# Kernel tuning notes

Hardware: AMD Instinct MI355X
Metric: run time of the kernel (lower is better)

The kernel has to match this reference:

```python
import jax, jax.numpy as jnp
import numpy as np

N_ACTIVE = 100000
C = 64
N_BLOCKS = 2
K = 27  # 3x3x3 submanifold rulebook offsets
BN_EPS = 1e-4  # scn BatchNorm default eps


def setup_inputs() -> dict:
    key = jax.random.key(0)
    k1, k2, k3 = jax.random.split(key, 3)
    feats = jax.random.normal(k1, (N_ACTIVE, C), dtype=jnp.float32)
    # rulebook: index N_ACTIVE == missing neighbor (points at padded zero row)
    nbrs = jax.random.randint(k2, (N_ACTIVE, K), 0, N_ACTIVE + 1, dtype=jnp.int32)
    # make the center offset (k=13) point at self, as in a real submanifold rulebook
    nbrs = nbrs.at[:, K // 2].set(jnp.arange(N_ACTIVE, dtype=jnp.int32))
    fan_in = K * C
    W = jax.random.normal(k3, (N_BLOCKS, 2, K, C, C), dtype=jnp.float32) / np.sqrt(fan_in)
    gamma = jnp.ones((N_BLOCKS, 2, C), dtype=jnp.float32)
    beta = jnp.zeros((N_BLOCKS, 2, C), dtype=jnp.float32)
    return {"feats": feats, "nbrs": nbrs, "W": W, "gamma": gamma, "beta": beta}


def _subm_conv(x, nbrs, Wk):
    # x: [N, C]; nbrs: [N, K] with value N meaning 'missing'; Wk: [K, C, C]
    x_pad = jnp.concatenate([x, jnp.zeros((1, x.shape[1]), x.dtype)], axis=0)
    g = x_pad[nbrs]  # [N, K, C] rulebook gather
    return jnp.einsum('nkc,kcd->nd', g, Wk)  # gather-GEMM-scatter fused by contraction


def _bn(x, g, b):
    mu = jnp.mean(x, axis=0)
    var = jnp.var(x, axis=0)
    return (x - mu) * jax.lax.rsqrt(var + BN_EPS) * g + b


def reference(feats, nbrs, W, gamma, beta):
    x = feats
    for i in range(N_BLOCKS):  # SparseResidualBlock chain
        residual = x
        out = _subm_conv(x, nbrs, W[i, 0])
        out = jax.nn.relu(_bn(out, gamma[i, 0], beta[i, 0]))  # BatchNormReLU
        out = _subm_conv(out, nbrs, W[i, 1])
        out = _bn(out, gamma[i, 1], beta[i, 1])  # BatchNormalization
        x = jax.nn.relu(out + residual)  # AddTable + ReLU
    return x
```

## Files before the change

### kernel.cpp

```cpp
#include <hip/hip_runtime.h>

#define N_PTS 100000
#define NT_STRIDE 100096
#define NK 27
#define TOTAL (N_PTS * 64)
#define NB_CONV 782

typedef short bf16x8 __attribute__((ext_vector_type(8)));
typedef float f32x4 __attribute__((ext_vector_type(4)));
typedef unsigned short u16x8 __attribute__((ext_vector_type(8)));

__device__ __forceinline__ unsigned short f2bf(float f) {
    unsigned u = __builtin_bit_cast(unsigned, f);
    u += 0x7fffu + ((u >> 16) & 1u);
    return (unsigned short)(u >> 16);
}
__device__ __forceinline__ float bf2f(unsigned short u) {
    return __builtin_bit_cast(float, ((unsigned)u) << 16);
}

__global__ void cast_in_k(const float* __restrict__ feats, unsigned short* __restrict__ xb) {
    int t = blockIdx.x * 256 + threadIdx.x;
    if (t >= (N_PTS + 1) * 8) return;
    int i = t * 8;
    u16x8 o;
    if (i < TOTAL) {
        f32x4 v0 = ((const f32x4*)(feats + i))[0];
        f32x4 v1 = ((const f32x4*)(feats + i))[1];
#pragma unroll
        for (int j = 0; j < 4; ++j) { o[j] = f2bf(v0[j]); o[4 + j] = f2bf(v1[j]); }
    } else {
#pragma unroll
        for (int j = 0; j < 8; ++j) o[j] = 0;
    }
    *(u16x8*)(xb + i) = o;
}

__global__ void tr_nbrs_k(const int* __restrict__ nbrs, int* __restrict__ nbrsT) {
    __shared__ int tile[64 * 28];
    const int n0 = blockIdx.x * 64;
    const int t = threadIdx.x;
    const int base = n0 * 27;
    for (int i = t; i < 1728; i += 256) {
        int v = (base + i < N_PTS * 27) ? nbrs[base + i] : N_PTS;
        int r = i / 27, c = i - r * 27;
        tile[r * 28 + c] = v;
    }
    __syncthreads();
    for (int i = t; i < 1728; i += 256) {
        int k = i >> 6, j = i & 63;
        nbrsT[(size_t)k * NT_STRIDE + n0 + j] = tile[j * 28 + k];
    }
}

__global__ void pack_w_k(const float* __restrict__ W, unsigned short* __restrict__ Wp) {
    int o = blockIdx.x * 256 + threadIdx.x;
    if (o >= 4 * NK * 4096) return;
    int conv = o / (NK * 4096);
    int r = o - conv * (NK * 4096);
    int k = r >> 12;
    int r2 = r & 4095;
    int frag = r2 >> 9;
    int kk = frag >> 2, cb = frag & 3;
    int lane = (r2 >> 3) & 63;
    int j = r2 & 7;
    int c = kk * 32 + (lane >> 4) * 8 + j;
    int d = cb * 16 + (lane & 15);
    Wp[o] = f2bf(W[(size_t)(conv * NK + k) * 4096 + c * 64 + d]);
}

__global__ __launch_bounds__(256, 3) void conv_k(
    const unsigned short* __restrict__ xb,
    const int* __restrict__ nbrsT,
    const unsigned short* __restrict__ Wp,
    unsigned short* __restrict__ ybf,
    float* __restrict__ partials)
{
    const int tid = threadIdx.x;
    const int lane = tid & 63;
    const int wave = tid >> 6;
    const int l15 = lane & 15;
    const int lgrp = lane >> 4;
    const int wave_row = blockIdx.x * 128 + wave * 32;
    const int r0 = wave_row + l15;
    const int r1 = r0 + 16;

    f32x4 acc[2][4];
#pragma unroll
    for (int m = 0; m < 2; ++m)
#pragma unroll
        for (int cb = 0; cb < 4; ++cb) acc[m][cb] = (f32x4)0.f;

    const bf16x8* wp = (const bf16x8*)Wp;

    int id0[4], id1[4];
#pragma unroll
    for (int s = 0; s < 4; ++s) {
        id0[s] = nbrsT[(size_t)s * NT_STRIDE + r0];
        id1[s] = nbrsT[(size_t)s * NT_STRIDE + r1];
    }
    bf16x8 apf[3][4];
#pragma unroll
    for (int s = 0; s < 2; ++s) {
        const bf16x8* p0 = (const bf16x8*)(xb + (size_t)id0[s] * 64);
        const bf16x8* p1 = (const bf16x8*)(xb + (size_t)id1[s] * 64);
        apf[s][0] = p0[lgrp]; apf[s][1] = p0[4 + lgrp];
        apf[s][2] = p1[lgrp]; apf[s][3] = p1[4 + lgrp];
    }

#pragma unroll
    for (int k = 0; k < NK; ++k) {
        if (k + 4 < NK) {
            id0[k & 3] = nbrsT[(size_t)(k + 4) * NT_STRIDE + r0];
            id1[k & 3] = nbrsT[(size_t)(k + 4) * NT_STRIDE + r1];
        }
        if (k + 2 < NK) {
            const int j = (k + 2) & 3;
            const int s2 = (k + 2) % 3;
            const bf16x8* p0 = (const bf16x8*)(xb + (size_t)id0[j] * 64);
            const bf16x8* p1 = (const bf16x8*)(xb + (size_t)id1[j] * 64);
            apf[s2][0] = p0[lgrp]; apf[s2][1] = p0[4 + lgrp];
            apf[s2][2] = p1[lgrp]; apf[s2][3] = p1[4 + lgrp];
        }
        const int s = k % 3;
        const bf16x8* wk = wp + (size_t)k * 512 + lane;
        {
            bf16x8 b0 = wk[0], b1 = wk[64], b2 = wk[128], b3 = wk[192];
            acc[0][0] = __builtin_amdgcn_mfma_f32_16x16x32_bf16(apf[s][0], b0, acc[0][0], 0, 0, 0);
            acc[1][0] = __builtin_amdgcn_mfma_f32_16x16x32_bf16(apf[s][2], b0, acc[1][0], 0, 0, 0);
            acc[0][1] = __builtin_amdgcn_mfma_f32_16x16x32_bf16(apf[s][0], b1, acc[0][1], 0, 0, 0);
            acc[1][1] = __builtin_amdgcn_mfma_f32_16x16x32_bf16(apf[s][2], b1, acc[1][1], 0, 0, 0);
            acc[0][2] = __builtin_amdgcn_mfma_f32_16x16x32_bf16(apf[s][0], b2, acc[0][2], 0, 0, 0);
            acc[1][2] = __builtin_amdgcn_mfma_f32_16x16x32_bf16(apf[s][2], b2, acc[1][2], 0, 0, 0);
            acc[0][3] = __builtin_amdgcn_mfma_f32_16x16x32_bf16(apf[s][0], b3, acc[0][3], 0, 0, 0);
            acc[1][3] = __builtin_amdgcn_mfma_f32_16x16x32_bf16(apf[s][2], b3, acc[1][3], 0, 0, 0);
        }
        {
            bf16x8 b0 = wk[256], b1 = wk[320], b2 = wk[384], b3 = wk[448];
            acc[0][0] = __builtin_amdgcn_mfma_f32_16x16x32_bf16(apf[s][1], b0, acc[0][0], 0, 0, 0);
            acc[1][0] = __builtin_amdgcn_mfma_f32_16x16x32_bf16(apf[s][3], b0, acc[1][0], 0, 0, 0);
            acc[0][1] = __builtin_amdgcn_mfma_f32_16x16x32_bf16(apf[s][1], b1, acc[0][1], 0, 0, 0);
            acc[1][1] = __builtin_amdgcn_mfma_f32_16x16x32_bf16(apf[s][3], b1, acc[1][1], 0, 0, 0);
            acc[0][2] = __builtin_amdgcn_mfma_f32_16x16x32_bf16(apf[s][1], b2, acc[0][2], 0, 0, 0);
            acc[1][2] = __builtin_amdgcn_mfma_f32_16x16x32_bf16(apf[s][3], b2, acc[1][2], 0, 0, 0);
            acc[0][3] = __builtin_amdgcn_mfma_f32_16x16x32_bf16(apf[s][1], b3, acc[0][3], 0, 0, 0);
            acc[1][3] = __builtin_amdgcn_mfma_f32_16x16x32_bf16(apf[s][3], b3, acc[1][3], 0, 0, 0);
        }
    }

    __shared__ __align__(16) unsigned short yt[4][32 * 72];
    unsigned short* myt = &yt[wave][0];
#pragma unroll
    for (int m = 0; m < 2; ++m)
#pragma unroll
        for (int cb = 0; cb < 4; ++cb)
#pragma unroll
            for (int r = 0; r < 4; ++r)
                myt[(m * 16 + lgrp * 4 + r) * 72 + cb * 16 + l15] = f2bf(acc[m][cb][r]);
#pragma unroll
    for (int c2 = 0; c2 < 4; ++c2) {
        int chunk = c2 * 64 + lane;
        int row = chunk >> 3;
        int col8 = chunk & 7;
        int grow = wave_row + row;
        if (grow < N_PTS) {
            u16x8 v = *(const u16x8*)(myt + row * 72 + col8 * 8);
            *(u16x8*)(ybf + (size_t)grow * 64 + col8 * 8) = v;
        }
    }

    __shared__ float sred[4][128];
#pragma unroll
    for (int cb = 0; cb < 4; ++cb) {
        float s = 0.f, s2 = 0.f;
#pragma unroll
        for (int m = 0; m < 2; ++m)
#pragma unroll
            for (int r = 0; r < 4; ++r) {
                float v = acc[m][cb][r];
                s += v; s2 += v * v;
            }
        s += __shfl_xor(s, 16); s += __shfl_xor(s, 32);
        s2 += __shfl_xor(s2, 16); s2 += __shfl_xor(s2, 32);
        if (lane < 16) {
            sred[wave][cb * 16 + l15] = s;
            sred[wave][64 + cb * 16 + l15] = s2;
        }
    }
    __syncthreads();
    if (tid < 128) {
        float p = sred[0][tid] + sred[1][tid] + sred[2][tid] + sred[3][tid];
        partials[(size_t)blockIdx.x * 128 + tid] = p;
    }
}

__global__ void bn_fin_k(const float* __restrict__ partials,
                         const float* __restrict__ gamma,
                         const float* __restrict__ beta,
                         float* __restrict__ scsh) {
    const int c = blockIdx.x;
    const int t = threadIdx.x;
    float s = 0.f, s2 = 0.f;
    for (int w = t; w < NB_CONV; w += 256) {
        s  += partials[(size_t)w * 128 + c];
        s2 += partials[(size_t)w * 128 + 64 + c];
    }
#pragma unroll
    for (int off = 1; off < 64; off <<= 1) {
        s  += __shfl_xor(s, off, 64);
        s2 += __shfl_xor(s2, off, 64);
    }
    __shared__ float sm[8];
    int wv = t >> 6, ln = t & 63;
    if (ln == 0) { sm[wv] = s; sm[4 + wv] = s2; }
    __syncthreads();
    if (t == 0) {
        float S  = sm[0] + sm[1] + sm[2] + sm[3];
        float S2 = sm[4] + sm[5] + sm[6] + sm[7];
        const float invN = 1.0f / (float)N_PTS;
        float mu = S * invN;
        float var = S2 * invN - mu * mu;
        float sc = gamma[c] * rsqrtf(var + 1e-4f);
        scsh[c] = sc;
        scsh[64 + c] = beta[c] - mu * sc;
    }
}

__global__ void bn_relu_cast_k(const unsigned short* __restrict__ ybf, const float* __restrict__ scsh,
                               unsigned short* __restrict__ xb) {
    int t = blockIdx.x * 256 + threadIdx.x;
    if (t >= TOTAL / 8) return;
    int i = t * 8;
    int c0 = i & 63;
    u16x8 v = *(const u16x8*)(ybf + i);
    f32x4 sa = *(const f32x4*)(scsh + c0);
    f32x4 sb = *(const f32x4*)(scsh + c0 + 4);
    f32x4 ba = *(const f32x4*)(scsh + 64 + c0);
    f32x4 bb = *(const f32x4*)(scsh + 64 + c0 + 4);
    u16x8 o;
#pragma unroll
    for (int j = 0; j < 4; ++j) {
        o[j]     = f2bf(fmaxf(bf2f(v[j])     * sa[j] + ba[j], 0.f));
        o[4 + j] = f2bf(fmaxf(bf2f(v[4 + j]) * sb[j] + bb[j], 0.f));
    }
    *(u16x8*)(xb + i) = o;
}

__global__ void bn_add_relu_k(const unsigned short* __restrict__ ybf, const float* __restrict__ scsh,
                              const float* __restrict__ res, float* __restrict__ xout,
                              unsigned short* __restrict__ xb, int writeBf) {
    int t = blockIdx.x * 256 + threadIdx.x;
    if (t >= TOTAL / 8) return;
    int i = t * 8;
    int c0 = i & 63;
    u16x8 v = *(const u16x8*)(ybf + i);
    f32x4 q0 = ((const f32x4*)(res + i))[0];
    f32x4 q1 = ((const f32x4*)(res + i))[1];
    f32x4 sa = *(const f32x4*)(scsh + c0);
    f32x4 sb = *(const f32x4*)(scsh + c0 + 4);
    f32x4 ba = *(const f32x4*)(scsh + 64 + c0);
    f32x4 bb = *(const f32x4*)(scsh + 64 + c0 + 4);
    f32x4 o0, o1;
#pragma unroll
    for (int j = 0; j < 4; ++j) {
        o0[j] = fmaxf(bf2f(v[j])     * sa[j] + ba[j] + q0[j], 0.f);
        o1[j] = fmaxf(bf2f(v[4 + j]) * sb[j] + bb[j] + q1[j], 0.f);
    }
    ((f32x4*)(xout + i))[0] = o0;
    ((f32x4*)(xout + i))[1] = o1;
    if (writeBf) {
        u16x8 o;
#pragma unroll
        for (int j = 0; j < 4; ++j) { o[j] = f2bf(o0[j]); o[4 + j] = f2bf(o1[j]); }
        *(u16x8*)(xb + i) = o;
    }
}

extern "C" void kernel_launch(void* const* d_in, const int* in_sizes, int n_in,
                              void* d_out, int out_size, void* d_ws, size_t ws_size,
                              hipStream_t stream) {
    const float* feats = (const float*)d_in[0];
    const int*   nbrs  = (const int*)d_in[1];
    const float* W     = (const float*)d_in[2];
    const float* gamma = (const float*)d_in[3];
    const float* beta  = (const float*)d_in[4];
    float* out = (float*)d_out;

    char* ws = (char*)d_ws;
    unsigned short* xb       = (unsigned short*)ws;
    unsigned short* ybf      = (unsigned short*)(ws + 12800512);
    unsigned short* Wp       = (unsigned short*)(ws + 25600512);
    int*            nbrsT    = (int*)(ws + 26485248);
    float*          partials = (float*)(ws + 37295616);
    float*          scsh     = (float*)(ws + 37696000);

    dim3 b256(256);
    cast_in_k<<<((N_PTS + 1) * 8 + 255) / 256, b256, 0, stream>>>(feats, xb);
    tr_nbrs_k<<<NT_STRIDE / 64, b256, 0, stream>>>(nbrs, nbrsT);
    pack_w_k<<<(4 * NK * 4096) / 256, b256, 0, stream>>>(W, Wp);

    const int appl_blocks = (TOTAL / 8) / 256;
    for (int blk = 0; blk < 2; ++blk) {
        int c0 = blk * 2, c1 = blk * 2 + 1;
        conv_k<<<NB_CONV, b256, 0, stream>>>(xb, nbrsT, Wp + (size_t)c0 * NK * 4096, ybf, partials);
        bn_fin_k<<<64, b256, 0, stream>>>(partials, gamma + c0 * 64, beta + c0 * 64, scsh);
        bn_relu_cast_k<<<appl_blocks, b256, 0, stream>>>(ybf, scsh, xb);
        conv_k<<<NB_CONV, b256, 0, stream>>>(xb, nbrsT, Wp + (size_t)c1 * NK * 4096, ybf, partials);
        bn_fin_k<<<64, b256, 0, stream>>>(partials, gamma + c1 * 64, beta + c1 * 64, scsh);
        const float* res = (blk == 0) ? feats : (const float*)out;
        bn_add_relu_k<<<appl_blocks, b256, 0, stream>>>(ybf, scsh, res, out, xb, blk == 0 ? 1 : 0);
    }
}
```

Measured before the change: 470.3 us.

## Split conv K-offsets across wave pairs with LDS reduction of partial sums

The conv kernel now gives each block 64 rows instead of 128, and splits the 27 offsets (padded to 28 with a zero weight slice and a missing-neighbor index row) between two wave pairs of 14 each. The two partial accumulators are combined through an fp32 LDS tile, after which all threads write bf16 output and compute the per-channel BN partial sums via shuffles. This doubles the grid and shortens each wave's serial gather/MFMA chain to expose more parallelism and latency hiding. In exchange it adds one padded offset of wasted work, extra LDS traffic and barriers, and twice as many partials for the BN finalize step. It also raises the launch-bounds occupancy hint and inserts a sched_barrier in the loop.

```diff
diff --git a/kernel.cpp b/kernel.cpp
--- a/kernel.cpp
+++ b/kernel.cpp
@@ -3,8 +3,9 @@
 #define N_PTS 100000
 #define NT_STRIDE 100096
 #define NK 27
+#define NKP 28
 #define TOTAL (N_PTS * 64)
-#define NB_CONV 782
+#define NB_CONV 1564
 
 typedef short bf16x8 __attribute__((ext_vector_type(8)));
 typedef float f32x4 __attribute__((ext_vector_type(4)));
@@ -51,14 +52,17 @@
         int k = i >> 6, j = i & 63;
         nbrsT[(size_t)k * NT_STRIDE + n0 + j] = tile[j * 28 + k];
     }
+    for (int i = t; i < 64; i += 256)
+        nbrsT[(size_t)27 * NT_STRIDE + n0 + i] = N_PTS;
 }
 
 __global__ void pack_w_k(const float* __restrict__ W, unsigned short* __restrict__ Wp) {
     int o = blockIdx.x * 256 + threadIdx.x;
-    if (o >= 4 * NK * 4096) return;
-    int conv = o / (NK * 4096);
-    int r = o - conv * (NK * 4096);
+    if (o >= 4 * NKP * 4096) return;
+    int conv = o / (NKP * 4096);
+    int r = o - conv * (NKP * 4096);
     int k = r >> 12;
+    if (k == 27) { Wp[o] = 0; return; }
     int r2 = r & 4095;
     int frag = r2 >> 9;
     int kk = frag >> 2, cb = frag & 3;
@@ -69,7 +73,7 @@
     Wp[o] = f2bf(W[(size_t)(conv * NK + k) * 4096 + c * 64 + d]);
 }
 
-__global__ __launch_bounds__(256, 3) void conv_k(
+__global__ __launch_bounds__(256, 4) void conv_k(
     const unsigned short* __restrict__ xb,
     const int* __restrict__ nbrsT,
     const unsigned short* __restrict__ Wp,
@@ -81,9 +85,12 @@
     const int wave = tid >> 6;
     const int l15 = lane & 15;
     const int lgrp = lane >> 4;
-    const int wave_row = blockIdx.x * 128 + wave * 32;
+    const int h = wave & 1;
+    const int kh = wave >> 1;
+    const int wave_row = blockIdx.x * 64 + h * 32;
     const int r0 = wave_row + l15;
     const int r1 = r0 + 16;
+    const int k0 = kh * 14;
 
     f32x4 acc[2][4];
 #pragma unroll
@@ -96,8 +103,8 @@
     int id0[4], id1[4];
 #pragma unroll
     for (int s = 0; s < 4; ++s) {
-        id0[s] = nbrsT[(size_t)s * NT_STRIDE + r0];
-        id1[s] = nbrsT[(size_t)s * NT_STRIDE + r1];
+        id0[s] = nbrsT[(size_t)(k0 + s) * NT_STRIDE + r0];
+        id1[s] = nbrsT[(size_t)(k0 + s) * NT_STRIDE + r1];
     }
     bf16x8 apf[3][4];
 #pragma unroll
@@ -109,82 +116,106 @@
     }
 
 #pragma unroll
-    for (int k = 0; k < NK; ++k) {
-        if (k + 4 < NK) {
-            id0[k & 3] = nbrsT[(size_t)(k + 4) * NT_STRIDE + r0];
-            id1[k & 3] = nbrsT[(size_t)(k + 4) * NT_STRIDE + r1];
-        }
-        if (k + 2 < NK) {
-            const int j = (k + 2) & 3;
-            const int s2 = (k + 2) % 3;
+    for (int s = 0; s < 14; ++s) {
+        if (s + 4 < 14) {
+            id0[s & 3] = nbrsT[(size_t)(k0 + s + 4) * NT_STRIDE + r0];
+            id1[s & 3] = nbrsT[(size_t)(k0 + s + 4) * NT_STRIDE + r1];
+        }
+        if (s + 2 < 14) {
+            const int j = (s + 2) & 3;
+            const int st = (s + 2) % 3;
             const bf16x8* p0 = (const bf16x8*)(xb + (size_t)id0[j] * 64);
             const bf16x8* p1 = (const bf16x8*)(xb + (size_t)id1[j] * 64);
-            apf[s2][0] = p0[lgrp]; apf[s2][1] = p0[4 + lgrp];
-            apf[s2][2] = p1[lgrp]; apf[s2][3] = p1[4 + lgrp];
-        }
-        const int s = k % 3;
-        const bf16x8* wk = wp + (size_t)k * 512 + lane;
+            apf[st][0] = p0[lgrp]; apf[st][1] = p0[4 + lgrp];
+            apf[st][2] = p1[lgrp]; apf[st][3] = p1[4 + lgrp];
+        }
+        __builtin_amdgcn_sched_barrier(0);
+        const int st = s % 3;
+        const bf16x8* wk = wp + (size_t)(k0 + s) * 512 + lane;
         {
             bf16x8 b0 = wk[0], b1 = wk[64], b2 = wk[128], b3 = wk[192];
-            acc[0][0] = __builtin_amdgcn_mfma_f32_16x16x32_bf16(apf[s][0], b0, acc[0][0], 0, 0, 0);
-            acc[1][0] = __builtin_amdgcn_mfma_f32_16x16x32_bf16(apf[s][2], b0, acc[1][0], 0, 0, 0);
-            acc[0][1] = __builtin_amdgcn_mfma_f32_16x16x32_bf16(apf[s][0], b1, acc[0][1], 0, 0, 0);
-            acc[1][1] = __builtin_amdgcn_mfma_f32_16x16x32_bf16(apf[s][2], b1, acc[1][1], 0, 0, 0);
-            acc[0][2] = __builtin_amdgcn_mfma_f32_16x16x32_bf16(apf[s][0], b2, acc[0][2], 0, 0, 0);
-            acc[1][2] = __builtin_amdgcn_mfma_f32_16x16x32_bf16(apf[s][2], b2, acc[1][2], 0, 0, 0);
-            acc[0][3] = __builtin_amdgcn_mfma_f32_16x16x32_bf16(apf[s][0], b3, acc[0][3], 0, 0, 0);
-            acc[1][3] = __builtin_amdgcn_mfma_f32_16x16x32_bf16(apf[s][2], b3, acc[1][3], 0, 0, 0);
+            acc[0][0] = __builtin_amdgcn_mfma_f32_16x16x32_bf16(apf[st][0], b0, acc[0][0], 0, 0, 0);
+            acc[1][0] = __builtin_amdgcn_mfma_f32_16x16x32_bf16(apf[st][2], b0, acc[1][0], 0, 0, 0);
+            acc[0][1] = __builtin_amdgcn_mfma_f32_16x16x32_bf16(apf[st][0], b1, acc[0][1], 0, 0, 0);
+            acc[1][1] = __builtin_amdgcn_mfma_f32_16x16x32_bf16(apf[st][2], b1, acc[1][1], 0, 0, 0);
+            acc[0][2] = __builtin_amdgcn_mfma_f32_16x16x32_bf16(apf[st][0], b2, acc[0][2], 0, 0, 0);
+            acc[1][2] = __builtin_amdgcn_mfma_f32_16x16x32_bf16(apf[st][2], b2, acc[1][2], 0, 0, 0);
+            acc[0][3] = __builtin_amdgcn_mfma_f32_16x16x32_bf16(apf[st][0], b3, acc[0][3], 0, 0, 0);
+            acc[1][3] = __builtin_amdgcn_mfma_f32_16x16x32_bf16(apf[st][2], b3, acc[1][3], 0, 0, 0);
         }
         {
             bf16x8 b0 = wk[256], b1 = wk[320], b2 = wk[384], b3 = wk[448];
-            acc[0][0] = __builtin_amdgcn_mfma_f32_16x16x32_bf16(apf[s][1], b0, acc[0][0], 0, 0, 0);
-            acc[1][0] = __builtin_amdgcn_mfma_f32_16x16x32_bf16(apf[s][3], b0, acc[1][0], 0, 0, 0);
-            acc[0][1] = __builtin_amdgcn_mfma_f32_16x16x32_bf16(apf[s][1], b1, acc[0][1], 0, 0, 0);
-            acc[1][1] = __builtin_amdgcn_mfma_f32_16x16x32_bf16(apf[s][3], b1, acc[1][1], 0, 0, 0);
-            acc[0][2] = __builtin_amdgcn_mfma_f32_16x16x32_bf16(apf[s][1], b2, acc[0][2], 0, 0, 0);
-            acc[1][2] = __builtin_amdgcn_mfma_f32_16x16x32_bf16(apf[s][3], b2, acc[1][2], 0, 0, 0);
-            acc[0][3] = __builtin_amdgcn_mfma_f32_16x16x32_bf16(apf[s][1], b3, acc[0][3], 0, 0, 0);
-            acc[1][3] = __builtin_amdgcn_mfma_f32_16x16x32_bf16(apf[s][3], b3, acc[1][3], 0, 0, 0);
-        }
-    }
-
-    __shared__ __align__(16) unsigned short yt[4][32 * 72];
-    unsigned short* myt = &yt[wave][0];
-#pragma unroll
-    for (int m = 0; m < 2; ++m)
-#pragma unroll
-        for (int cb = 0; cb < 4; ++cb)
-#pragma unroll
-            for (int r = 0; r < 4; ++r)
-                myt[(m * 16 + lgrp * 4 + r) * 72 + cb * 16 + l15] = f2bf(acc[m][cb][r]);
-#pragma unroll
-    for (int c2 = 0; c2 < 4; ++c2) {
-        int chunk = c2 * 64 + lane;
-        int row = chunk >> 3;
-        int col8 = chunk & 7;
-        int grow = wave_row + row;
-        if (grow < N_PTS) {
-            u16x8 v = *(const u16x8*)(myt + row * 72 + col8 * 8);
-            *(u16x8*)(ybf + (size_t)grow * 64 + col8 * 8) = v;
-        }
-    }
-
-    __shared__ float sred[4][128];
-#pragma unroll
-    for (int cb = 0; cb < 4; ++cb) {
-        float s = 0.f, s2 = 0.f;
+            acc[0][0] = __builtin_amdgcn_mfma_f32_16x16x32_bf16(apf[st][1], b0, acc[0][0], 0, 0, 0);
+            acc[1][0] = __builtin_amdgcn_mfma_f32_16x16x32_bf16(apf[st][3], b0, acc[1][0], 0, 0, 0);
+            acc[0][1] = __builtin_amdgcn_mfma_f32_16x16x32_bf16(apf[st][1], b1, acc[0][1], 0, 0, 0);
+            acc[1][1] = __builtin_amdgcn_mfma_f32_16x16x32_bf16(apf[st][3], b1, acc[1][1], 0, 0, 0);
+            acc[0][2] = __builtin_amdgcn_mfma_f32_16x16x32_bf16(apf[st][1], b2, acc[0][2], 0, 0, 0);
+            acc[1][2] = __builtin_amdgcn_mfma_f32_16x16x32_bf16(apf[st][3], b2, acc[1][2], 0, 0, 0);
+            acc[0][3] = __builtin_amdgcn_mfma_f32_16x16x32_bf16(apf[st][1], b3, acc[0][3], 0, 0, 0);
+            acc[1][3] = __builtin_amdgcn_mfma_f32_16x16x32_bf16(apf[st][3], b3, acc[1][3], 0, 0, 0);
+        }
+    }
+
+    __shared__ __align__(16) float ytile[64 * 68];
+    __shared__ __align__(16) float sred[4][128];
+
+    if (kh == 0) {
 #pragma unroll
         for (int m = 0; m < 2; ++m)
 #pragma unroll
-            for (int r = 0; r < 4; ++r) {
-                float v = acc[m][cb][r];
-                s += v; s2 += v * v;
+            for (int cb = 0; cb < 4; ++cb)
+#pragma unroll
+                for (int r = 0; r < 4; ++r)
+                    ytile[(h * 32 + m * 16 + lgrp * 4 + r) * 68 + cb * 16 + l15] = acc[m][cb][r];
+    }
+    __syncthreads();
+    if (kh == 1) {
+#pragma unroll
+        for (int m = 0; m < 2; ++m)
+#pragma unroll
+            for (int cb = 0; cb < 4; ++cb)
+#pragma unroll
+                for (int r = 0; r < 4; ++r)
+                    ytile[(h * 32 + m * 16 + lgrp * 4 + r) * 68 + cb * 16 + l15] += acc[m][cb][r];
+    }
+    __syncthreads();
+
+    const int row = tid >> 2;
+    const int colb = (tid & 3) * 16;
+    f32x4 v[4];
+#pragma unroll
+    for (int j = 0; j < 4; ++j) v[j] = *(const f32x4*)&ytile[row * 68 + colb + 4 * j];
+
+    const int grow = blockIdx.x * 64 + row;
+    if (grow < N_PTS) {
+        u16x8 o0, o1;
+#pragma unroll
+        for (int j = 0; j < 4; ++j) { o0[j] = f2bf(v[0][j]); o0[4 + j] = f2bf(v[1][j]); }
+#pragma unroll
+        for (int j = 0; j < 4; ++j) { o1[j] = f2bf(v[2][j]); o1[4 + j] = f2bf(v[3][j]); }
+        *(u16x8*)(ybf + (size_t)grow * 64 + colb) = o0;
+        *(u16x8*)(ybf + (size_t)grow * 64 + colb + 8) = o1;
+    }
+
+    f32x4 sv[4], s2v[4];
+#pragma unroll
+    for (int j = 0; j < 4; ++j) { sv[j] = v[j]; s2v[j] = v[j] * v[j]; }
+#pragma unroll
+    for (int off = 4; off < 64; off <<= 1) {
+#pragma unroll
+        for (int j = 0; j < 4; ++j) {
+#pragma unroll
+            for (int e = 0; e < 4; ++e) {
+                sv[j][e]  += __shfl_xor(sv[j][e],  off);
+                s2v[j][e] += __shfl_xor(s2v[j][e], off);
             }
-        s += __shfl_xor(s, 16); s += __shfl_xor(s, 32);
-        s2 += __shfl_xor(s2, 16); s2 += __shfl_xor(s2, 32);
-        if (lane < 16) {
-            sred[wave][cb * 16 + l15] = s;
-            sred[wave][64 + cb * 16 + l15] = s2;
+        }
+    }
+    if (lane < 4) {
+#pragma unroll
+        for (int j = 0; j < 4; ++j) {
+            *(f32x4*)&sred[wave][lane * 16 + 4 * j]      = sv[j];
+            *(f32x4*)&sred[wave][64 + lane * 16 + 4 * j] = s2v[j];
         }
     }
     __syncthreads();
@@ -211,8 +242,8 @@
         s2 += __shfl_xor(s2, off, 64);
     }
     __shared__ float sm[8];
-    int wv = t >> 6, ln = t & 63;
-    if (ln == 0) { sm[wv] = s; sm[4 + wv] = s2; }
+    int wv = t >> 6;
+    if ((t & 63) == 0) { sm[wv] = s; sm[4 + wv] = s2; }
     __syncthreads();
     if (t == 0) {
         float S  = sm[0] + sm[1] + sm[2] + sm[3];
@@ -290,22 +321,22 @@
     unsigned short* xb       = (unsigned short*)ws;
     unsigned short* ybf      = (unsigned short*)(ws + 12800512);
     unsigned short* Wp       = (unsigned short*)(ws + 25600512);
-    int*            nbrsT    = (int*)(ws + 26485248);
-    float*          partials = (float*)(ws + 37295616);
-    float*          scsh     = (float*)(ws + 37696000);
+    int*            nbrsT    = (int*)(ws + 26518016);
+    float*          partials = (float*)(ws + 37728768);
+    float*          scsh     = (float*)(ws + 38529536);
 
     dim3 b256(256);
     cast_in_k<<<((N_PTS + 1) * 8 + 255) / 256, b256, 0, stream>>>(feats, xb);
     tr_nbrs_k<<<NT_STRIDE / 64, b256, 0, stream>>>(nbrs, nbrsT);
-    pack_w_k<<<(4 * NK * 4096) / 256, b256, 0, stream>>>(W, Wp);
+    pack_w_k<<<(4 * NKP * 4096) / 256, b256, 0, stream>>>(W, Wp);
 
     const int appl_blocks = (TOTAL / 8) / 256;
     for (int blk = 0; blk < 2; ++blk) {
         int c0 = blk * 2, c1 = blk * 2 + 1;
-        conv_k<<<NB_CONV, b256, 0, stream>>>(xb, nbrsT, Wp + (size_t)c0 * NK * 4096, ybf, partials);
+        conv_k<<<NB_CONV, b256, 0, stream>>>(xb, nbrsT, Wp + (size_t)c0 * NKP * 4096, ybf, partials);
         bn_fin_k<<<64, b256, 0, stream>>>(partials, gamma + c0 * 64, beta + c0 * 64, scsh);
         bn_relu_cast_k<<<appl_blocks, b256, 0, stream>>>(ybf, scsh, xb);
-        conv_k<<<NB_CONV, b256, 0, stream>>>(xb, nbrsT, Wp + (size_t)c1 * NK * 4096, ybf, partials);
+        conv_k<<<NB_CONV, b256, 0, stream>>>(xb, nbrsT, Wp + (size_t)c1 * NKP * 4096, ybf, partials);
         bn_fin_k<<<64, b256, 0, stream>>>(partials, gamma + c1 * 64, beta + c1 * 64, scsh);
         const float* res = (blk == 0) ? feats : (const float*)out;
         bn_add_relu_k<<<appl_blocks, b256, 0, stream>>>(ybf, scsh, res, out, xb, blk == 0 ? 1 : 0);
```

New measurement: 472.8 us. Within noise of the previous version (+0.5%).
